# Kernel tuning notes

Measured on AMD Instinct MI355X. Metric: run time of the kernel, lower is better.

Reference implementation:

```python
import jax, jax.numpy as jnp
import numpy as np

EMBED_DIM = 512
NUM_HEADS = 8
HEAD_DIM = EMBED_DIM // NUM_HEADS
B, S = 4, 2048


def setup_inputs() -> dict:
    key = jax.random.key(0)
    ks = jax.random.split(key, 9)
    scale = 1.0 / np.sqrt(EMBED_DIM)
    def lin(k):
        kw, kb = jax.random.split(k)
        W = jax.random.uniform(kw, (EMBED_DIM, EMBED_DIM), jnp.float32, -scale, scale)
        b = jax.random.uniform(kb, (EMBED_DIM,), jnp.float32, -scale, scale)
        return W, b
    Wq, bq = lin(ks[0])
    Wk, bk = lin(ks[1])
    Wv, bv = lin(ks[2])
    Wo, bo = lin(ks[3])
    x = jax.random.normal(ks[4], (B, S, EMBED_DIM), jnp.float32)
    return {"x": x, "Wq": Wq, "bq": bq, "Wk": Wk, "bk": bk,
            "Wv": Wv, "bv": bv, "Wo": Wo, "bo": bo}


def reference(x, Wq, bq, Wk, bk, Wv, bv, Wo, bo):
    # x: [B, S, E]. Linear uses y = x @ W^T + b (torch convention: W stored [out,in]).
    def split_heads(t):
        return t.reshape(B, S, NUM_HEADS, HEAD_DIM).transpose(0, 2, 1, 3)  # [B,H,S,D]
    q = split_heads(x @ Wq.T + bq)
    k = split_heads(x @ Wk.T + bk)
    v = split_heads(x @ Wv.T + bv)
    scores = jnp.einsum('bhsd,bhtd->bhst', q, k) / jnp.sqrt(jnp.float32(HEAD_DIM))
    attn_weights = jax.nn.softmax(scores, axis=-1)  # dropout is identity in eval mode
    attn_output = jnp.einsum('bhst,bhtd->bhsd', attn_weights, v)
    attn_output = attn_output.transpose(0, 2, 1, 3).reshape(B, S, EMBED_DIM)
    output = attn_output @ Wo.T + bo
    return output, attn_weights
```

## Files before the change

### kernel.cpp

```cpp
#include <hip/hip_runtime.h>
#include <stdint.h>

#define NB 4
#define NH 8
#define SS 2048
#define EE 512
#define DD 64
#define MM (NB*SS)
#define LDP 72
#define LDW 136

typedef __attribute__((ext_vector_type(8))) __bf16 bf16x8;
typedef __attribute__((ext_vector_type(8))) unsigned short ushort8;
typedef __attribute__((ext_vector_type(4))) unsigned short ushort4v;
typedef __attribute__((ext_vector_type(4))) float f32x4;

__device__ __forceinline__ uint16_t f2bf(float f) {
    union { float f; uint32_t u; } v; v.f = f;
    return (uint16_t)((v.u + 0x7fffu + ((v.u >> 16) & 1u)) >> 16);
}
__device__ __forceinline__ float bf2f(uint16_t h) {
    union { uint32_t u; float f; } v; v.u = ((uint32_t)h) << 16;
    return v.f;
}

__global__ __launch_bounds__(256) void split_all(
        const float* __restrict__ x,  const float* __restrict__ Wq,
        const float* __restrict__ Wk, const float* __restrict__ Wv,
        const float* __restrict__ Wo,
        uint16_t* __restrict__ xh, uint16_t* __restrict__ xl,
        uint16_t* __restrict__ wqkvh, uint16_t* __restrict__ wqkvl,
        uint16_t* __restrict__ woh, uint16_t* __restrict__ wol)
{
    const int tid = threadIdx.x;
    int b = blockIdx.x;
    const float* src; uint16_t* dh; uint16_t* dl; int i;
    if (b < 4096) { src = x; dh = xh; dl = xl; i = b*256 + tid; }
    else {
        b -= 4096;
        const int seg = b >> 8;
        i = (b & 255)*256 + tid;
        src = (seg == 0) ? Wq : (seg == 1) ? Wk : (seg == 2) ? Wv : Wo;
        if (seg < 3) { dh = wqkvh + (size_t)seg*262144; dl = wqkvl + (size_t)seg*262144; }
        else         { dh = woh; dl = wol; }
    }
    f32x4 v = reinterpret_cast<const f32x4*>(src)[i];
    ushort4v h, l;
#pragma unroll
    for (int j = 0; j < 4; j++) {
        uint16_t hh = f2bf(v[j]);
        h[j] = hh;
        l[j] = f2bf(v[j] - bf2f(hh));
    }
    reinterpret_cast<ushort4v*>(dh)[i] = h;
    reinterpret_cast<ushort4v*>(dl)[i] = l;
}

__global__ __launch_bounds__(256, 2)
void gemm_qkv(const uint16_t* __restrict__ Ah, const uint16_t* __restrict__ Al,
              const uint16_t* __restrict__ Bh, const uint16_t* __restrict__ Bl,
              const float* __restrict__ bq, const float* __restrict__ bk,
              const float* __restrict__ bv, float qscale,
              uint16_t* __restrict__ qh, uint16_t* __restrict__ ql,
              uint16_t* __restrict__ kh, uint16_t* __restrict__ kl,
              uint16_t* __restrict__ vh)
{
    __shared__ uint16_t sAh[64*LDP], sAl[64*LDP], sBh[128*LDP], sBl[128*LDP];
    const int t = threadIdx.x;
    const int lane = t & 63;
    const int wave = t >> 6;
    const int m0 = blockIdx.x * 64;
    const int n0 = blockIdx.y * 128;

    f32x4 zero = {0.f, 0.f, 0.f, 0.f};
    f32x4 acc[2][4];
#pragma unroll
    for (int i = 0; i < 2; i++)
#pragma unroll
        for (int j = 0; j < 4; j++) acc[i][j] = zero;

    const int sr = t >> 3;
    const int sc = (t & 7) * 8;

    for (int k0 = 0; k0 < EE; k0 += 64) {
#pragma unroll
        for (int p = 0; p < 2; p++) {
            const int row = sr + 32 * p;
            const size_t ga = (size_t)(m0 + row) * EE + k0 + sc;
            *reinterpret_cast<ushort8*>(&sAh[row*LDP + sc]) = *reinterpret_cast<const ushort8*>(&Ah[ga]);
            *reinterpret_cast<ushort8*>(&sAl[row*LDP + sc]) = *reinterpret_cast<const ushort8*>(&Al[ga]);
        }
#pragma unroll
        for (int p = 0; p < 4; p++) {
            const int row = sr + 32 * p;
            const size_t gb = (size_t)(n0 + row) * EE + k0 + sc;
            *reinterpret_cast<ushort8*>(&sBh[row*LDP + sc]) = *reinterpret_cast<const ushort8*>(&Bh[gb]);
            *reinterpret_cast<ushort8*>(&sBl[row*LDP + sc]) = *reinterpret_cast<const ushort8*>(&Bl[gb]);
        }
        __syncthreads();
        const int mw = (wave >> 1) * 32;
        const int nw = (wave & 1) * 64;
#pragma unroll
        for (int ks = 0; ks < 2; ks++) {
            const int kk = ks*32 + (lane >> 4) * 8;
            bf16x8 fah[2], fal[2], fbh[4], fbl[4];
#pragma unroll
            for (int i = 0; i < 2; i++) {
                const int ra = (mw + 16*i + (lane & 15)) * LDP + kk;
                fah[i] = *reinterpret_cast<const bf16x8*>(&sAh[ra]);
                fal[i] = *reinterpret_cast<const bf16x8*>(&sAl[ra]);
            }
#pragma unroll
            for (int j = 0; j < 4; j++) {
                const int rb = (nw + 16*j + (lane & 15)) * LDP + kk;
                fbh[j] = *reinterpret_cast<const bf16x8*>(&sBh[rb]);
                fbl[j] = *reinterpret_cast<const bf16x8*>(&sBl[rb]);
            }
#pragma unroll
            for (int i = 0; i < 2; i++)
#pragma unroll
                for (int j = 0; j < 4; j++) {
                    acc[i][j] = __builtin_amdgcn_mfma_f32_16x16x32_bf16(fah[i], fbh[j], acc[i][j], 0, 0, 0);
                    acc[i][j] = __builtin_amdgcn_mfma_f32_16x16x32_bf16(fah[i], fbl[j], acc[i][j], 0, 0, 0);
                    acc[i][j] = __builtin_amdgcn_mfma_f32_16x16x32_bf16(fal[i], fbh[j], acc[i][j], 0, 0, 0);
                }
        }
        __syncthreads();
    }

    const int mw = (wave >> 1) * 32;
    const int nw = (wave & 1) * 64;
#pragma unroll
    for (int j = 0; j < 4; j++) {
        const int col = n0 + nw + 16*j + (lane & 15);
        const int seg = col >> 9;
        const int c   = col & 511;
        const float bias = (seg == 0 ? bq : (seg == 1 ? bk : bv))[c];
        const float scale = (seg == 0) ? qscale : 1.0f;
        const int h = c >> 6, d = c & 63;
#pragma unroll
        for (int i = 0; i < 2; i++) {
            const int rowb = m0 + mw + 16*i + ((lane >> 4) << 2);
#pragma unroll
            for (int r4 = 0; r4 < 4; r4++) {
                const int m = rowb + r4;
                const float val = (acc[i][j][r4] + bias) * scale;
                const int bb = m >> 11, s = m & (SS-1);
                const size_t idx = (((size_t)(bb*NH + h)) * SS + s) * DD + d;
                const uint16_t hi = f2bf(val);
                if (seg == 0)      { qh[idx] = hi; ql[idx] = f2bf(val - bf2f(hi)); }
                else if (seg == 1) { kh[idx] = hi; kl[idx] = f2bf(val - bf2f(hi)); }
                else               { vh[idx] = hi; }
            }
        }
    }
}

__global__ __launch_bounds__(256, 2)
void gemm_out(const uint16_t* __restrict__ Ah, const uint16_t* __restrict__ Al,
              const uint16_t* __restrict__ Bh, const uint16_t* __restrict__ Bl,
              const float* __restrict__ bo, float* __restrict__ Of)
{
    __shared__ uint16_t sAh[64*LDP], sAl[64*LDP], sBh[128*LDP], sBl[128*LDP];
    const int t = threadIdx.x;
    const int lane = t & 63;
    const int wave = t >> 6;
    const int m0 = blockIdx.x * 64;
    const int n0 = blockIdx.y * 128;

    f32x4 zero = {0.f, 0.f, 0.f, 0.f};
    f32x4 acc[2][4];
#pragma unroll
    for (int i = 0; i < 2; i++)
#pragma unroll
        for (int j = 0; j < 4; j++) acc[i][j] = zero;

    const int sr = t >> 3;
    const int sc = (t & 7) * 8;

    for (int k0 = 0; k0 < EE; k0 += 64) {
#pragma unroll
        for (int p = 0; p < 2; p++) {
            const int row = sr + 32 * p;
            const size_t ga = (size_t)(m0 + row) * EE + k0 + sc;
            *reinterpret_cast<ushort8*>(&sAh[row*LDP + sc]) = *reinterpret_cast<const ushort8*>(&Ah[ga]);
            *reinterpret_cast<ushort8*>(&sAl[row*LDP + sc]) = *reinterpret_cast<const ushort8*>(&Al[ga]);
        }
#pragma unroll
        for (int p = 0; p < 4; p++) {
            const int row = sr + 32 * p;
            const size_t gb = (size_t)(n0 + row) * EE + k0 + sc;
            *reinterpret_cast<ushort8*>(&sBh[row*LDP + sc]) = *reinterpret_cast<const ushort8*>(&Bh[gb]);
            *reinterpret_cast<ushort8*>(&sBl[row*LDP + sc]) = *reinterpret_cast<const ushort8*>(&Bl[gb]);
        }
        __syncthreads();
        const int mw = (wave >> 1) * 32;
        const int nw = (wave & 1) * 64;
#pragma unroll
        for (int ks = 0; ks < 2; ks++) {
            const int kk = ks*32 + (lane >> 4) * 8;
            bf16x8 fah[2], fal[2], fbh[4], fbl[4];
#pragma unroll
            for (int i = 0; i < 2; i++) {
                const int ra = (mw + 16*i + (lane & 15)) * LDP + kk;
                fah[i] = *reinterpret_cast<const bf16x8*>(&sAh[ra]);
                fal[i] = *reinterpret_cast<const bf16x8*>(&sAl[ra]);
            }
#pragma unroll
            for (int j = 0; j < 4; j++) {
                const int rb = (nw + 16*j + (lane & 15)) * LDP + kk;
                fbh[j] = *reinterpret_cast<const bf16x8*>(&sBh[rb]);
                fbl[j] = *reinterpret_cast<const bf16x8*>(&sBl[rb]);
            }
#pragma unroll
            for (int i = 0; i < 2; i++)
#pragma unroll
                for (int j = 0; j < 4; j++) {
                    acc[i][j] = __builtin_amdgcn_mfma_f32_16x16x32_bf16(fah[i], fbh[j], acc[i][j], 0, 0, 0);
                    acc[i][j] = __builtin_amdgcn_mfma_f32_16x16x32_bf16(fah[i], fbl[j], acc[i][j], 0, 0, 0);
                    acc[i][j] = __builtin_amdgcn_mfma_f32_16x16x32_bf16(fal[i], fbh[j], acc[i][j], 0, 0, 0);
                }
        }
        __syncthreads();
    }

    const int mw = (wave >> 1) * 32;
    const int nw = (wave & 1) * 64;
#pragma unroll
    for (int j = 0; j < 4; j++) {
        const int col = n0 + nw + 16*j + (lane & 15);
        const float bv = bo[col];
#pragma unroll
        for (int i = 0; i < 2; i++) {
            const int rowb = m0 + mw + 16*i + ((lane >> 4) << 2);
#pragma unroll
            for (int r4 = 0; r4 < 4; r4++)
                Of[(size_t)(rowb + r4) * EE + col] = acc[i][j][r4] + bv;
        }
    }
}

__global__ __launch_bounds__(256, 2)
void attn_fused(const uint16_t* __restrict__ Qh, const uint16_t* __restrict__ Ql,
                const uint16_t* __restrict__ Kh, const uint16_t* __restrict__ Kl,
                const uint16_t* __restrict__ Vh,
                float* __restrict__ attn,
                uint16_t* __restrict__ Oh, uint16_t* __restrict__ Ol)
{
    __shared__ __align__(16) uint16_t smem[36864];
    uint16_t* bufA = smem;
    uint16_t* bufB = smem + 18432;

    const int t = threadIdx.x, lane = t & 63, wave = t >> 6;
    const int qt = blockIdx.x, bh = blockIdx.y;
    const size_t hb = (size_t)bh * SS * DD;
    const uint16_t* kbh = Kh + hb;
    const uint16_t* kbl = Kl + hb;
    const uint16_t* vbs = Vh + hb;

    const int l15 = lane & 15;
    const int l16 = lane >> 4;
    const int sr = t >> 3;
    const int sc = (t & 7) * 8;

    ushort8 krh[4], krl[4];
    auto kload_hi = [&](int kt) {
#pragma unroll
        for (int p = 0; p < 4; p++) {
            const size_t g = (size_t)(kt*128 + sr + 32*p) * DD + sc;
            krh[p] = *reinterpret_cast<const ushort8*>(&kbh[g]);
        }
    };
    auto kwrite_hi = [&](uint16_t* buf) {
#pragma unroll
        for (int p = 0; p < 4; p++) {
            const int o = (sr + 32*p)*LDP + sc;
            *reinterpret_cast<ushort8*>(&buf[o]) = krh[p];
        }
    };
    auto kload = [&](int kt) {
#pragma unroll
        for (int p = 0; p < 4; p++) {
            const size_t g = (size_t)(kt*128 + sr + 32*p) * DD + sc;
            krh[p] = *reinterpret_cast<const ushort8*>(&kbh[g]);
            krl[p] = *reinterpret_cast<const ushort8*>(&kbl[g]);
        }
    };
    auto kwrite = [&](uint16_t* buf) {
#pragma unroll
        for (int p = 0; p < 4; p++) {
            const int o = (sr + 32*p)*LDP + sc;
            *reinterpret_cast<ushort8*>(&buf[o]) = krh[p];
            *reinterpret_cast<ushort8*>(&buf[9216 + o]) = krl[p];
        }
    };

    bf16x8 qfh[2][2], qfl[2][2];
#pragma unroll
    for (int i = 0; i < 2; i++)
#pragma unroll
        for (int ks = 0; ks < 2; ks++) {
            const size_t qa = hb + (size_t)(qt*128 + wave*32 + 16*i + l15) * DD + ks*32 + l16*8;
            qfh[i][ks] = *reinterpret_cast<const bf16x8*>(&Qh[qa]);
            qfl[i][ks] = *reinterpret_cast<const bf16x8*>(&Ql[qa]);
        }

    f32x4 zero = {0.f, 0.f, 0.f, 0.f};
    f32x4 lsum[2] = {zero, zero};

    kload_hi(0);
#pragma unroll 1
    for (int kt = 0; kt < 16; kt++) {
        uint16_t* buf = (kt & 1) ? bufB : bufA;
        kwrite_hi(buf);
        if (kt < 15) kload_hi(kt + 1);
        __syncthreads();

        f32x4 accs[2][8];
#pragma unroll
        for (int i = 0; i < 2; i++)
#pragma unroll
            for (int j = 0; j < 8; j++) accs[i][j] = zero;

#pragma unroll
        for (int ks = 0; ks < 2; ks++) {
            const int kk = ks*32 + l16*8;
#pragma unroll
            for (int j = 0; j < 8; j++) {
                const int rb = (16*j + l15) * LDP + kk;
                bf16x8 fbh = *reinterpret_cast<const bf16x8*>(&buf[rb]);
#pragma unroll
                for (int i = 0; i < 2; i++)
                    accs[i][j] = __builtin_amdgcn_mfma_f32_16x16x32_bf16(qfh[i][ks], fbh, accs[i][j], 0, 0, 0);
            }
        }

#pragma unroll
        for (int i = 0; i < 2; i++)
#pragma unroll
            for (int j = 0; j < 8; j++)
#pragma unroll
                for (int r = 0; r < 4; r++)
                    lsum[i][r] += __builtin_amdgcn_exp2f(accs[i][j][r]);
    }

    f32x4 iv[2];
#pragma unroll
    for (int i = 0; i < 2; i++)
#pragma unroll
        for (int r = 0; r < 4; r++) {
            float s = lsum[i][r];
#pragma unroll
            for (int o = 1; o < 16; o <<= 1) s += __shfl_xor(s, o);
            iv[i][r] = 1.0f / s;
        }

    f32x4 acco[2][4];
#pragma unroll
    for (int i = 0; i < 2; i++)
#pragma unroll
        for (int j = 0; j < 4; j++) acco[i][j] = zero;

    float* wbase = attn + ((size_t)bh * SS + qt*128) * SS;

    const int pk = t & 63;
    const int dbase = (t >> 6) * 16;
    ushort8 vr[2][2];
    auto vload = [&](int kt) {
#pragma unroll
        for (int u = 0; u < 2; u++)
#pragma unroll
            for (int s = 0; s < 2; s++)
                vr[u][s] = *reinterpret_cast<const ushort8*>(
                    &vbs[(size_t)(kt*128 + 2*pk + s) * DD + dbase + u*8]);
    };
    auto vwrite = [&]() {
#pragma unroll
        for (int u = 0; u < 2; u++)
#pragma unroll
            for (int e = 0; e < 8; e++) {
                const int d = dbase + u*8 + e;
                const uint32_t pack = (uint32_t)(unsigned short)vr[u][0][e]
                                    | ((uint32_t)(unsigned short)vr[u][1][e] << 16);
                *reinterpret_cast<uint32_t*>(&bufB[d*LDW + 2*pk]) = pack;
            }
    };

    __syncthreads();

    kload(0); vload(0);
#pragma unroll 1
    for (int kt = 0; kt < 16; kt++) {
        kwrite(bufA);
        vwrite();
        __syncthreads();

        f32x4 accs[2][8];
#pragma unroll
        for (int i = 0; i < 2; i++)
#pragma unroll
            for (int j = 0; j < 8; j++) accs[i][j] = zero;
#pragma unroll
        for (int ks = 0; ks < 2; ks++) {
            const int kk = ks*32 + l16*8;
#pragma unroll
            for (int j = 0; j < 8; j++) {
                const int rb = (16*j + l15) * LDP + kk;
                bf16x8 fbh = *reinterpret_cast<const bf16x8*>(&bufA[rb]);
                bf16x8 fbl = *reinterpret_cast<const bf16x8*>(&bufA[9216 + rb]);
#pragma unroll
                for (int i = 0; i < 2; i++) {
                    accs[i][j] = __builtin_amdgcn_mfma_f32_16x16x32_bf16(qfh[i][ks], fbh, accs[i][j], 0, 0, 0);
                    accs[i][j] = __builtin_amdgcn_mfma_f32_16x16x32_bf16(qfh[i][ks], fbl, accs[i][j], 0, 0, 0);
                    accs[i][j] = __builtin_amdgcn_mfma_f32_16x16x32_bf16(qfl[i][ks], fbh, accs[i][j], 0, 0, 0);
                }
            }
        }

        if (kt < 15) { kload(kt + 1); vload(kt + 1); }

#pragma unroll
        for (int i = 0; i < 2; i++)
#pragma unroll
            for (int j = 0; j < 8; j++)
#pragma unroll
                for (int r = 0; r < 4; r++)
                    accs[i][j][r] = __builtin_amdgcn_exp2f(accs[i][j][r]) * iv[i][r];

        __syncthreads();

#pragma unroll
        for (int i = 0; i < 2; i++)
#pragma unroll
            for (int r = 0; r < 4; r++) {
                const int row = wave*32 + 16*i + l16*4 + r;
#pragma unroll
                for (int j = 0; j < 8; j++)
                    bufA[row*LDW + l15 + 16*j] = f2bf(accs[i][j][r]);
            }
        __syncthreads();

#pragma unroll
        for (int i = 0; i < 2; i++)
#pragma unroll
            for (int r = 0; r < 4; r++) {
                const int row = wave*32 + 16*i + l16*4 + r;
                float* wout = wbase + (size_t)row * SS + kt*128 + l15;
#pragma unroll
                for (int j = 0; j < 8; j++) wout[16*j] = accs[i][j][r];
            }

#pragma unroll
        for (int ks = 0; ks < 4; ks++) {
            const int kk = ks*32 + l16*8;
            bf16x8 wa[2], vbf[4];
#pragma unroll
            for (int i = 0; i < 2; i++)
                wa[i] = *reinterpret_cast<const bf16x8*>(&bufA[(wave*32 + 16*i + l15)*LDW + kk]);
#pragma unroll
            for (int j = 0; j < 4; j++)
                vbf[j] = *reinterpret_cast<const bf16x8*>(&bufB[(16*j + l15)*LDW + kk]);
#pragma unroll
            for (int i = 0; i < 2; i++)
#pragma unroll
                for (int j = 0; j < 4; j++)
                    acco[i][j] = __builtin_amdgcn_mfma_f32_16x16x32_bf16(wa[i], vbf[j], acco[i][j], 0, 0, 0);
        }
        __syncthreads();
    }

    const int b = bh >> 3, h = bh & 7;
#pragma unroll
    for (int i = 0; i < 2; i++)
#pragma unroll
        for (int j = 0; j < 4; j++)
#pragma unroll
            for (int r4 = 0; r4 < 4; r4++) {
                const int srow = qt*128 + wave*32 + 16*i + (l16 << 2) + r4;
                const int col = h*64 + 16*j + l15;
                const size_t idx = ((size_t)b * SS + srow) * (size_t)EE + col;
                const float val = acco[i][j][r4];
                const uint16_t hh = f2bf(val);
                Oh[idx] = hh;
                Ol[idx] = f2bf(val - bf2f(hh));
            }
}

extern "C" void kernel_launch(void* const* d_in, const int* in_sizes, int n_in,
                              void* d_out, int out_size, void* d_ws, size_t ws_size,
                              hipStream_t stream)
{
    const float* x  = (const float*)d_in[0];
    const float* Wq = (const float*)d_in[1];
    const float* bq = (const float*)d_in[2];
    const float* Wk = (const float*)d_in[3];
    const float* bk = (const float*)d_in[4];
    const float* Wv = (const float*)d_in[5];
    const float* bv = (const float*)d_in[6];
    const float* Wo = (const float*)d_in[7];
    const float* bo = (const float*)d_in[8];

    float* outF = (float*)d_out;
    float* attn = outF + (size_t)MM * EE;

    const size_t NXE = (size_t)MM * EE;
    const size_t NW  = (size_t)EE * EE;
    uint16_t* p = (uint16_t*)d_ws;
    uint16_t* xh    = p;          p += NXE;
    uint16_t* xl    = p;          p += NXE;
    uint16_t* wqkvh = p;          p += 3*NW;
    uint16_t* wqkvl = p;          p += 3*NW;
    uint16_t* woh   = p;          p += NW;
    uint16_t* wol   = p;          p += NW;
    uint16_t* qh    = p;          p += NXE;
    uint16_t* ql    = p;          p += NXE;
    uint16_t* kh    = p;          p += NXE;
    uint16_t* kl    = p;          p += NXE;
    uint16_t* vh    = p;          p += NXE;
    uint16_t* ah    = p;          p += NXE;
    uint16_t* al    = p;          p += NXE;

    split_all<<<4096 + 4*256, 256, 0, stream>>>(x, Wq, Wk, Wv, Wo,
                                                xh, xl, wqkvh, wqkvl, woh, wol);

    const float qscale = 0.125f * 1.44269504088896340736f;
    gemm_qkv<<<dim3(MM/64, (3*EE)/128), 256, 0, stream>>>(
        xh, xl, wqkvh, wqkvl, bq, bk, bv, qscale, qh, ql, kh, kl, vh);

    attn_fused<<<dim3(SS/128, NB*NH), 256, 0, stream>>>(qh, ql, kh, kl, vh, attn, ah, al);

    gemm_out<<<dim3(MM/64, EE/128), 256, 0, stream>>>(ah, al, woh, wol, bo, outF);
}
```

Measured before the change: 257.3 us.

## Replace padded LDS layouts with XOR-swizzled layouts and split attention buffers

Drops the padded row strides in the GEMM and attention kernels and uses XOR-swizzled 16-byte chunk layouts in LDS, so tiles fit with less shared memory while avoiding bank conflicts. The GEMM kernels raise launch bounds from 2 to 3 blocks per CU to use the smaller LDS footprint. The attention kernel gets separate regions for K, the probability tile and V, which removes one barrier before the probability write. The trade-offs are tighter register limits from the higher occupancy target and extra address arithmetic for the swizzles.

```diff
diff --git a/kernel.cpp b/kernel.cpp
--- a/kernel.cpp
+++ b/kernel.cpp
@@ -7,8 +7,6 @@
 #define EE 512
 #define DD 64
 #define MM (NB*SS)
-#define LDP 72
-#define LDW 136
 
 typedef __attribute__((ext_vector_type(8))) __bf16 bf16x8;
 typedef __attribute__((ext_vector_type(8))) unsigned short ushort8;
@@ -56,7 +54,7 @@
     reinterpret_cast<ushort4v*>(dl)[i] = l;
 }
 
-__global__ __launch_bounds__(256, 2)
+__global__ __launch_bounds__(256, 3)
 void gemm_qkv(const uint16_t* __restrict__ Ah, const uint16_t* __restrict__ Al,
               const uint16_t* __restrict__ Bh, const uint16_t* __restrict__ Bl,
               const float* __restrict__ bq, const float* __restrict__ bk,
@@ -65,7 +63,7 @@
               uint16_t* __restrict__ kh, uint16_t* __restrict__ kl,
               uint16_t* __restrict__ vh)
 {
-    __shared__ uint16_t sAh[64*LDP], sAl[64*LDP], sBh[128*LDP], sBl[128*LDP];
+    __shared__ uint16_t sAh[64*64], sAl[64*64], sBh[128*64], sBl[128*64];
     const int t = threadIdx.x;
     const int lane = t & 63;
     const int wave = t >> 6;
@@ -80,39 +78,47 @@
         for (int j = 0; j < 4; j++) acc[i][j] = zero;
 
     const int sr = t >> 3;
-    const int sc = (t & 7) * 8;
+    const int c8 = t & 7;
+    const int sc = c8 * 8;
+    const int dsw = ((c8 ^ (sr & 7)) << 3);
+    const int l15 = lane & 15;
+    const int l16 = lane >> 4;
 
     for (int k0 = 0; k0 < EE; k0 += 64) {
 #pragma unroll
         for (int p = 0; p < 2; p++) {
             const int row = sr + 32 * p;
             const size_t ga = (size_t)(m0 + row) * EE + k0 + sc;
-            *reinterpret_cast<ushort8*>(&sAh[row*LDP + sc]) = *reinterpret_cast<const ushort8*>(&Ah[ga]);
-            *reinterpret_cast<ushort8*>(&sAl[row*LDP + sc]) = *reinterpret_cast<const ushort8*>(&Al[ga]);
+            const int o = row*64 + dsw;
+            *reinterpret_cast<ushort8*>(&sAh[o]) = *reinterpret_cast<const ushort8*>(&Ah[ga]);
+            *reinterpret_cast<ushort8*>(&sAl[o]) = *reinterpret_cast<const ushort8*>(&Al[ga]);
         }
 #pragma unroll
         for (int p = 0; p < 4; p++) {
             const int row = sr + 32 * p;
             const size_t gb = (size_t)(n0 + row) * EE + k0 + sc;
-            *reinterpret_cast<ushort8*>(&sBh[row*LDP + sc]) = *reinterpret_cast<const ushort8*>(&Bh[gb]);
-            *reinterpret_cast<ushort8*>(&sBl[row*LDP + sc]) = *reinterpret_cast<const ushort8*>(&Bl[gb]);
+            const int o = row*64 + dsw;
+            *reinterpret_cast<ushort8*>(&sBh[o]) = *reinterpret_cast<const ushort8*>(&Bh[gb]);
+            *reinterpret_cast<ushort8*>(&sBl[o]) = *reinterpret_cast<const ushort8*>(&Bl[gb]);
         }
         __syncthreads();
         const int mw = (wave >> 1) * 32;
         const int nw = (wave & 1) * 64;
 #pragma unroll
         for (int ks = 0; ks < 2; ks++) {
-            const int kk = ks*32 + (lane >> 4) * 8;
+            const int kc = ks*4 + l16;
             bf16x8 fah[2], fal[2], fbh[4], fbl[4];
 #pragma unroll
             for (int i = 0; i < 2; i++) {
-                const int ra = (mw + 16*i + (lane & 15)) * LDP + kk;
+                const int ar = mw + 16*i + l15;
+                const int ra = ar*64 + ((kc ^ (ar & 7)) << 3);
                 fah[i] = *reinterpret_cast<const bf16x8*>(&sAh[ra]);
                 fal[i] = *reinterpret_cast<const bf16x8*>(&sAl[ra]);
             }
 #pragma unroll
             for (int j = 0; j < 4; j++) {
-                const int rb = (nw + 16*j + (lane & 15)) * LDP + kk;
+                const int br = nw + 16*j + l15;
+                const int rb = br*64 + ((kc ^ (br & 7)) << 3);
                 fbh[j] = *reinterpret_cast<const bf16x8*>(&sBh[rb]);
                 fbl[j] = *reinterpret_cast<const bf16x8*>(&sBl[rb]);
             }
@@ -132,7 +138,7 @@
     const int nw = (wave & 1) * 64;
 #pragma unroll
     for (int j = 0; j < 4; j++) {
-        const int col = n0 + nw + 16*j + (lane & 15);
+        const int col = n0 + nw + 16*j + l15;
         const int seg = col >> 9;
         const int c   = col & 511;
         const float bias = (seg == 0 ? bq : (seg == 1 ? bk : bv))[c];
@@ -140,7 +146,7 @@
         const int h = c >> 6, d = c & 63;
 #pragma unroll
         for (int i = 0; i < 2; i++) {
-            const int rowb = m0 + mw + 16*i + ((lane >> 4) << 2);
+            const int rowb = m0 + mw + 16*i + (l16 << 2);
 #pragma unroll
             for (int r4 = 0; r4 < 4; r4++) {
                 const int m = rowb + r4;
@@ -156,12 +162,12 @@
     }
 }
 
-__global__ __launch_bounds__(256, 2)
+__global__ __launch_bounds__(256, 3)
 void gemm_out(const uint16_t* __restrict__ Ah, const uint16_t* __restrict__ Al,
               const uint16_t* __restrict__ Bh, const uint16_t* __restrict__ Bl,
               const float* __restrict__ bo, float* __restrict__ Of)
 {
-    __shared__ uint16_t sAh[64*LDP], sAl[64*LDP], sBh[128*LDP], sBl[128*LDP];
+    __shared__ uint16_t sAh[64*64], sAl[64*64], sBh[128*64], sBl[128*64];
     const int t = threadIdx.x;
     const int lane = t & 63;
     const int wave = t >> 6;
@@ -176,39 +182,47 @@
         for (int j = 0; j < 4; j++) acc[i][j] = zero;
 
     const int sr = t >> 3;
-    const int sc = (t & 7) * 8;
+    const int c8 = t & 7;
+    const int sc = c8 * 8;
+    const int dsw = ((c8 ^ (sr & 7)) << 3);
+    const int l15 = lane & 15;
+    const int l16 = lane >> 4;
 
     for (int k0 = 0; k0 < EE; k0 += 64) {
 #pragma unroll
         for (int p = 0; p < 2; p++) {
             const int row = sr + 32 * p;
             const size_t ga = (size_t)(m0 + row) * EE + k0 + sc;
-            *reinterpret_cast<ushort8*>(&sAh[row*LDP + sc]) = *reinterpret_cast<const ushort8*>(&Ah[ga]);
-            *reinterpret_cast<ushort8*>(&sAl[row*LDP + sc]) = *reinterpret_cast<const ushort8*>(&Al[ga]);
+            const int o = row*64 + dsw;
+            *reinterpret_cast<ushort8*>(&sAh[o]) = *reinterpret_cast<const ushort8*>(&Ah[ga]);
+            *reinterpret_cast<ushort8*>(&sAl[o]) = *reinterpret_cast<const ushort8*>(&Al[ga]);
         }
 #pragma unroll
         for (int p = 0; p < 4; p++) {
             const int row = sr + 32 * p;
             const size_t gb = (size_t)(n0 + row) * EE + k0 + sc;
-            *reinterpret_cast<ushort8*>(&sBh[row*LDP + sc]) = *reinterpret_cast<const ushort8*>(&Bh[gb]);
-            *reinterpret_cast<ushort8*>(&sBl[row*LDP + sc]) = *reinterpret_cast<const ushort8*>(&Bl[gb]);
+            const int o = row*64 + dsw;
+            *reinterpret_cast<ushort8*>(&sBh[o]) = *reinterpret_cast<const ushort8*>(&Bh[gb]);
+            *reinterpret_cast<ushort8*>(&sBl[o]) = *reinterpret_cast<const ushort8*>(&Bl[gb]);
         }
         __syncthreads();
         const int mw = (wave >> 1) * 32;
         const int nw = (wave & 1) * 64;
 #pragma unroll
         for (int ks = 0; ks < 2; ks++) {
-            const int kk = ks*32 + (lane >> 4) * 8;
+            const int kc = ks*4 + l16;
             bf16x8 fah[2], fal[2], fbh[4], fbl[4];
 #pragma unroll
             for (int i = 0; i < 2; i++) {
-                const int ra = (mw + 16*i + (lane & 15)) * LDP + kk;
+                const int ar = mw + 16*i + l15;
+                const int ra = ar*64 + ((kc ^ (ar & 7)) << 3);
                 fah[i] = *reinterpret_cast<const bf16x8*>(&sAh[ra]);
                 fal[i] = *reinterpret_cast<const bf16x8*>(&sAl[ra]);
             }
 #pragma unroll
             for (int j = 0; j < 4; j++) {
-                const int rb = (nw + 16*j + (lane & 15)) * LDP + kk;
+                const int br = nw + 16*j + l15;
+                const int rb = br*64 + ((kc ^ (br & 7)) << 3);
                 fbh[j] = *reinterpret_cast<const bf16x8*>(&sBh[rb]);
                 fbl[j] = *reinterpret_cast<const bf16x8*>(&sBl[rb]);
             }
@@ -228,11 +242,11 @@
     const int nw = (wave & 1) * 64;
 #pragma unroll
     for (int j = 0; j < 4; j++) {
-        const int col = n0 + nw + 16*j + (lane & 15);
+        const int col = n0 + nw + 16*j + l15;
         const float bv = bo[col];
 #pragma unroll
         for (int i = 0; i < 2; i++) {
-            const int rowb = m0 + mw + 16*i + ((lane >> 4) << 2);
+            const int rowb = m0 + mw + 16*i + (l16 << 2);
 #pragma unroll
             for (int r4 = 0; r4 < 4; r4++)
                 Of[(size_t)(rowb + r4) * EE + col] = acc[i][j][r4] + bv;
@@ -247,9 +261,10 @@
                 float* __restrict__ attn,
                 uint16_t* __restrict__ Oh, uint16_t* __restrict__ Ol)
 {
-    __shared__ __align__(16) uint16_t smem[36864];
-    uint16_t* bufA = smem;
-    uint16_t* bufB = smem + 18432;
+    __shared__ __align__(16) uint16_t smem[40960];
+    uint16_t* kreg = smem;
+    uint16_t* wlds = smem + 16384;
+    uint16_t* vlds = smem + 32768;
 
     const int t = threadIdx.x, lane = t & 63, wave = t >> 6;
     const int qt = blockIdx.x, bh = blockIdx.y;
@@ -261,22 +276,20 @@
     const int l15 = lane & 15;
     const int l16 = lane >> 4;
     const int sr = t >> 3;
-    const int sc = (t & 7) * 8;
+    const int c8 = t & 7;
+    const int sc = c8 * 8;
+    const int dsw = ((c8 ^ (sr & 7)) << 3);
 
     ushort8 krh[4], krl[4];
     auto kload_hi = [&](int kt) {
 #pragma unroll
-        for (int p = 0; p < 4; p++) {
-            const size_t g = (size_t)(kt*128 + sr + 32*p) * DD + sc;
-            krh[p] = *reinterpret_cast<const ushort8*>(&kbh[g]);
-        }
+        for (int p = 0; p < 4; p++)
+            krh[p] = *reinterpret_cast<const ushort8*>(&kbh[(size_t)(kt*128 + sr + 32*p) * DD + sc]);
     };
     auto kwrite_hi = [&](uint16_t* buf) {
 #pragma unroll
-        for (int p = 0; p < 4; p++) {
-            const int o = (sr + 32*p)*LDP + sc;
-            *reinterpret_cast<ushort8*>(&buf[o]) = krh[p];
-        }
+        for (int p = 0; p < 4; p++)
+            *reinterpret_cast<ushort8*>(&buf[(sr + 32*p)*64 + dsw]) = krh[p];
     };
     auto kload = [&](int kt) {
 #pragma unroll
@@ -286,12 +299,12 @@
             krl[p] = *reinterpret_cast<const ushort8*>(&kbl[g]);
         }
     };
-    auto kwrite = [&](uint16_t* buf) {
+    auto kwrite = [&]() {
 #pragma unroll
         for (int p = 0; p < 4; p++) {
-            const int o = (sr + 32*p)*LDP + sc;
-            *reinterpret_cast<ushort8*>(&buf[o]) = krh[p];
-            *reinterpret_cast<ushort8*>(&buf[9216 + o]) = krl[p];
+            const int o = (sr + 32*p)*64 + dsw;
+            *reinterpret_cast<ushort8*>(&kreg[o]) = krh[p];
+            *reinterpret_cast<ushort8*>(&kreg[8192 + o]) = krl[p];
         }
     };
 
@@ -311,7 +324,7 @@
     kload_hi(0);
 #pragma unroll 1
     for (int kt = 0; kt < 16; kt++) {
-        uint16_t* buf = (kt & 1) ? bufB : bufA;
+        uint16_t* buf = kreg + (kt & 1) * 8192;
         kwrite_hi(buf);
         if (kt < 15) kload_hi(kt + 1);
         __syncthreads();
@@ -324,11 +337,11 @@
 
 #pragma unroll
         for (int ks = 0; ks < 2; ks++) {
-            const int kk = ks*32 + l16*8;
+            const int kc = ks*4 + l16;
 #pragma unroll
             for (int j = 0; j < 8; j++) {
-                const int rb = (16*j + l15) * LDP + kk;
-                bf16x8 fbh = *reinterpret_cast<const bf16x8*>(&buf[rb]);
+                const int kr = 16*j + l15;
+                bf16x8 fbh = *reinterpret_cast<const bf16x8*>(&buf[kr*64 + ((kc ^ (kr & 7)) << 3)]);
 #pragma unroll
                 for (int i = 0; i < 2; i++)
                     accs[i][j] = __builtin_amdgcn_mfma_f32_16x16x32_bf16(qfh[i][ks], fbh, accs[i][j], 0, 0, 0);
@@ -380,9 +393,10 @@
 #pragma unroll
             for (int e = 0; e < 8; e++) {
                 const int d = dbase + u*8 + e;
+                const int off = d*128 + (((pk >> 2) ^ (d & 7)) << 3) + 2*(pk & 3);
                 const uint32_t pack = (uint32_t)(unsigned short)vr[u][0][e]
                                     | ((uint32_t)(unsigned short)vr[u][1][e] << 16);
-                *reinterpret_cast<uint32_t*>(&bufB[d*LDW + 2*pk]) = pack;
+                *reinterpret_cast<uint32_t*>(&vlds[off]) = pack;
             }
     };
 
@@ -391,7 +405,7 @@
     kload(0); vload(0);
 #pragma unroll 1
     for (int kt = 0; kt < 16; kt++) {
-        kwrite(bufA);
+        kwrite();
         vwrite();
         __syncthreads();
 
@@ -402,12 +416,13 @@
             for (int j = 0; j < 8; j++) accs[i][j] = zero;
 #pragma unroll
         for (int ks = 0; ks < 2; ks++) {
-            const int kk = ks*32 + l16*8;
+            const int kc = ks*4 + l16;
 #pragma unroll
             for (int j = 0; j < 8; j++) {
-                const int rb = (16*j + l15) * LDP + kk;
-                bf16x8 fbh = *reinterpret_cast<const bf16x8*>(&bufA[rb]);
-                bf16x8 fbl = *reinterpret_cast<const bf16x8*>(&bufA[9216 + rb]);
+                const int kr = 16*j + l15;
+                const int rb = kr*64 + ((kc ^ (kr & 7)) << 3);
+                bf16x8 fbh = *reinterpret_cast<const bf16x8*>(&kreg[rb]);
+                bf16x8 fbl = *reinterpret_cast<const bf16x8*>(&kreg[8192 + rb]);
 #pragma unroll
                 for (int i = 0; i < 2; i++) {
                     accs[i][j] = __builtin_amdgcn_mfma_f32_16x16x32_bf16(qfh[i][ks], fbh, accs[i][j], 0, 0, 0);
@@ -427,16 +442,17 @@
                 for (int r = 0; r < 4; r++)
                     accs[i][j][r] = __builtin_amdgcn_exp2f(accs[i][j][r]) * iv[i][r];
 
-        __syncthreads();
-
 #pragma unroll
         for (int i = 0; i < 2; i++)
 #pragma unroll
             for (int r = 0; r < 4; r++) {
                 const int row = wave*32 + 16*i + l16*4 + r;
-#pragma unroll
-                for (int j = 0; j < 8; j++)
-                    bufA[row*LDW + l15 + 16*j] = f2bf(accs[i][j][r]);
+                const int rm = row & 7;
+#pragma unroll
+                for (int j = 0; j < 8; j++) {
+                    const int off = row*128 + ((((2*j + (l15 >> 3)) ^ rm)) << 3) + (l15 & 7);
+                    wlds[off] = f2bf(accs[i][j][r]);
+                }
             }
         __syncthreads();
 
@@ -452,14 +468,18 @@
 
 #pragma unroll
         for (int ks = 0; ks < 4; ks++) {
-            const int kk = ks*32 + l16*8;
+            const int kc = ks*4 + l16;
             bf16x8 wa[2], vbf[4];
 #pragma unroll
-            for (int i = 0; i < 2; i++)
-                wa[i] = *reinterpret_cast<const bf16x8*>(&bufA[(wave*32 + 16*i + l15)*LDW + kk]);
-#pragma unroll
-            for (int j = 0; j < 4; j++)
-                vbf[j] = *reinterpret_cast<const bf16x8*>(&bufB[(16*j + l15)*LDW + kk]);
+            for (int i = 0; i < 2; i++) {
+                const int row = wave*32 + 16*i + l15;
+                wa[i] = *reinterpret_cast<const bf16x8*>(&wlds[row*128 + ((kc ^ (row & 7)) << 3)]);
+            }
+#pragma unroll
+            for (int j = 0; j < 4; j++) {
+                const int d = 16*j + l15;
+                vbf[j] = *reinterpret_cast<const bf16x8*>(&vlds[d*128 + ((kc ^ (d & 7)) << 3)]);
+            }
 #pragma unroll
             for (int i = 0; i < 2; i++)
 #pragma unroll
```

New measurement: 496.2 us. 1.93x slower.
